# Optimization experiments

Measured on AMD Instinct MI355X. Metric: run time of the kernel, lower is better.

Reference implementation:

```python
import jax, jax.numpy as jnp
import numpy as np

ENC = 512            # encoder_image_size
RADIUS = 5.0         # user_input_circle_radius
B, Q, P = 4, 8, 4
IN_H, IN_W = 1024, 1024


def setup_inputs() -> dict:
    key = jax.random.key(0)
    k1, k2, k3 = jax.random.split(key, 3)
    batched_images = jax.random.uniform(k1, (B, 3, IN_H, IN_W), dtype=jnp.float32)
    # points in pixel coordinates of the input image
    batched_points = jax.random.uniform(k2, (B, Q, P, 2), dtype=jnp.float32) * jnp.float32(IN_W)
    batched_point_labels = jax.random.randint(k3, (B, Q, P), 0, 4, dtype=jnp.int32)
    pixel_mean = jnp.array([0.485, 0.456, 0.406], dtype=jnp.float32).reshape(1, 3, 1, 1)
    pixel_std = jnp.array([0.229, 0.224, 0.225], dtype=jnp.float32).reshape(1, 3, 1, 1)
    return {
        "batched_images": batched_images,
        "batched_points": batched_points,
        "batched_point_labels": batched_point_labels,
        "pixel_mean": pixel_mean,
        "pixel_std": pixel_std,
    }


def _early_fusion(batched_images, batched_points, batched_point_labels, pixel_mean, pixel_std):
    b, _, in_h, in_w = batched_images.shape
    q = batched_points.shape[1]
    S = ENC
    # preprocess: bilinear resize (align_corners=False) + normalize
    x = jax.image.resize(batched_images, (b, 3, S, S), method="bilinear", antialias=False)
    x = (x - pixel_mean) / pixel_std
    # rescale points to encoder resolution, keeping negatives at -1
    px = jnp.where(batched_points[..., 0] >= 0, batched_points[..., 0] * (S / in_w), -1.0)
    py = jnp.where(batched_points[..., 1] >= 0, batched_points[..., 1] * (S / in_h), -1.0)
    pts = jnp.stack([px, py], axis=-1)                      # [B,Q,P,2]

    rows = jnp.arange(S, dtype=jnp.float32)                 # row ids (y)
    cols = jnp.arange(S, dtype=jnp.float32)                 # col ids (x)

    # bbox mask from first two points if label[...,0] != 1, else full image
    is_bbox = (batched_point_labels[:, :, 0] != 1).astype(jnp.float32)   # [B,Q]
    tlx = is_bbox * jnp.min(pts[:, :, :2, 0], axis=-1)
    tly = is_bbox * jnp.min(pts[:, :, :2, 1], axis=-1)
    brx = is_bbox * jnp.max(pts[:, :, :2, 0], axis=-1) + (1.0 - is_bbox) * S
    bry = is_bbox * jnp.max(pts[:, :, :2, 1], axis=-1) + (1.0 - is_bbox) * S
    row_within = (rows[None, None, :, None] >= tly[:, :, None, None]) & (rows[None, None, :, None] <= bry[:, :, None, None])
    col_within = (cols[None, None, None, :] >= tlx[:, :, None, None]) & (cols[None, None, None, :] <= brx[:, :, None, None])
    bbox_mask = (row_within & col_within).astype(x.dtype)   # [B,Q,S,S]

    # point (circle) mask: min over points of squared distance, gated by label==1
    is_point = (batched_point_labels == 1).astype(jnp.float32)[:, :, None, None, :]   # [B,Q,1,1,P]
    dx = cols[None, None, None, :, None] - pts[:, :, None, None, :, 0]  # [B,Q,1,S,P]
    dy = rows[None, None, :, None, None] - pts[:, :, None, None, :, 1]  # [B,Q,S,1,P]
    d2 = dx * dx + dy * dy                                               # [B,Q,S,S,P]
    r2 = RADIUS * RADIUS
    gated = d2 * is_point + (1.0 - is_point) * (r2 + 1.0)
    pts_mask = (jnp.min(gated, axis=-1) <= r2).astype(x.dtype)          # [B,Q,S,S]

    imgs = jnp.broadcast_to(x[:, None], (b, q, 3, S, S))
    fused = jnp.concatenate([imgs, bbox_mask[:, :, None], pts_mask[:, :, None]], axis=2)
    return fused.reshape(b * q, 5, S, S)


def reference(batched_images, batched_points, batched_point_labels, pixel_mean, pixel_std):
    return _early_fusion(batched_images, batched_points, batched_point_labels, pixel_mean, pixel_std)
```

## Files before the change

### kernel.cpp

```cpp
#include <hip/hip_runtime.h>

#define S_ENC 512
#define IN_WH 1024
#define NB 4
#define NQ 8
#define NPTS 4

__global__ __launch_bounds__(256) void resize_norm_kernel(
    const float* __restrict__ img,
    const float* __restrict__ mean,
    const float* __restrict__ stdv,
    float* __restrict__ wimg)
{
  const int bc  = blockIdx.y;
  const int tid = blockIdx.x * 256 + threadIdx.x;
  const int y   = tid >> 7;
  const int x4  = (tid & 127) << 2;

  const float m = mean[bc % 3];
  const float s = stdv[bc % 3];

  const float* in0 = img + ((size_t)bc * IN_WH + (size_t)(2 * y)) * IN_WH + 2 * x4;
  const float4 a0 = *(const float4*)(in0);
  const float4 a1 = *(const float4*)(in0 + 4);
  const float4 b0 = *(const float4*)(in0 + IN_WH);
  const float4 b1 = *(const float4*)(in0 + IN_WH + 4);

  float4 r;
  r.x = 0.5f * (0.5f * (a0.x + a0.y) + 0.5f * (b0.x + b0.y));
  r.y = 0.5f * (0.5f * (a0.z + a0.w) + 0.5f * (b0.z + b0.w));
  r.z = 0.5f * (0.5f * (a1.x + a1.y) + 0.5f * (b1.x + b1.y));
  r.w = 0.5f * (0.5f * (a1.z + a1.w) + 0.5f * (b1.z + b1.w));
  r.x = (r.x - m) / s;
  r.y = (r.y - m) / s;
  r.z = (r.z - m) / s;
  r.w = (r.w - m) / s;

  *(float4*)(wimg + ((size_t)bc * S_ENC + y) * S_ENC + x4) = r;
}

template <bool UseWs>
__global__ __launch_bounds__(256) void fuse_kernel(
    const float* __restrict__ wimg,
    const float* __restrict__ img,
    const float* __restrict__ pts,
    const int*   __restrict__ labels,
    const float* __restrict__ mean,
    const float* __restrict__ stdv,
    float* __restrict__ out)
{
  const int plane = blockIdx.y;
  const int c  = plane % 5;
  const int bq = plane / 5;
  const int b  = bq >> 3;
  const int q  = bq & 7;

  const int tid = blockIdx.x * 256 + threadIdx.x;
  const int y   = tid >> 7;
  const int x4  = (tid & 127) << 2;

  float4 r;

  if (c < 3) {
    if (UseWs) {
      r = *(const float4*)(wimg + ((size_t)(b * 3 + c) * S_ENC + y) * S_ENC + x4);
    } else {
      const float m = mean[c];
      const float s = stdv[c];
      const float* in0 =
          img + ((size_t)(b * 3 + c) * IN_WH + (size_t)(2 * y)) * IN_WH + 2 * x4;
      const float4 a0 = *(const float4*)(in0);
      const float4 a1 = *(const float4*)(in0 + 4);
      const float4 b0 = *(const float4*)(in0 + IN_WH);
      const float4 b1 = *(const float4*)(in0 + IN_WH + 4);
      r.x = 0.5f * (0.5f * (a0.x + a0.y) + 0.5f * (b0.x + b0.y));
      r.y = 0.5f * (0.5f * (a0.z + a0.w) + 0.5f * (b0.z + b0.w));
      r.z = 0.5f * (0.5f * (a1.x + a1.y) + 0.5f * (b1.x + b1.y));
      r.w = 0.5f * (0.5f * (a1.z + a1.w) + 0.5f * (b1.z + b1.w));
      r.x = (r.x - m) / s;
      r.y = (r.y - m) / s;
      r.z = (r.z - m) / s;
      r.w = (r.w - m) / s;
    }
  } else {
    const float* p   = pts + (size_t)(bq) * NPTS * 2;
    const int*   lab = labels + (size_t)(bq) * NPTS;
    float px[NPTS], py[NPTS];
    int   lb[NPTS];
#pragma unroll
    for (int i = 0; i < NPTS; ++i) {
      const float vx = p[2 * i + 0];
      const float vy = p[2 * i + 1];
      px[i] = (vx >= 0.0f) ? __fmul_rn(vx, 0.5f) : -1.0f;
      py[i] = (vy >= 0.0f) ? __fmul_rn(vy, 0.5f) : -1.0f;
      lb[i] = lab[i];
    }
    const float fy = (float)y;
    float* rr = &r.x;

    if (c == 3) {
      float tlx, tly, brx, bry;
      if (lb[0] != 1) {
        tlx = fminf(px[0], px[1]);
        tly = fminf(py[0], py[1]);
        brx = fmaxf(px[0], px[1]);
        bry = fmaxf(py[0], py[1]);
      } else {
        tlx = 0.0f; tly = 0.0f;
        brx = (float)S_ENC; bry = (float)S_ENC;
      }
      const bool rowok = (fy >= tly) && (fy <= bry);
#pragma unroll
      for (int j = 0; j < 4; ++j) {
        const float fx = (float)(x4 + j);
        rr[j] = (rowok && fx >= tlx && fx <= brx) ? 1.0f : 0.0f;
      }
    } else {
#pragma unroll
      for (int j = 0; j < 4; ++j) {
        const float fx = (float)(x4 + j);
        float mind = 26.0f;
#pragma unroll
        for (int i = 0; i < NPTS; ++i) {
          if (lb[i] == 1) {
            const float dx = __fsub_rn(fx, px[i]);
            const float dy = __fsub_rn(fy, py[i]);
            const float d2 = __fadd_rn(__fmul_rn(dx, dx), __fmul_rn(dy, dy));
            mind = fminf(mind, d2);
          }
        }
        rr[j] = (mind <= 25.0f) ? 1.0f : 0.0f;
      }
    }
  }

  *(float4*)(out + ((size_t)plane * S_ENC + y) * S_ENC + x4) = r;
}

extern "C" void kernel_launch(void* const* d_in, const int* in_sizes, int n_in,
                              void* d_out, int out_size, void* d_ws, size_t ws_size,
                              hipStream_t stream) {
  const float* img    = (const float*)d_in[0];
  const float* pts    = (const float*)d_in[1];
  const int*   labels = (const int*)d_in[2];
  const float* mean   = (const float*)d_in[3];
  const float* stdv   = (const float*)d_in[4];
  float* out = (float*)d_out;

  const size_t ws_need = (size_t)NB * 3 * S_ENC * S_ENC * sizeof(float);

  if (d_ws != nullptr && ws_size >= ws_need) {
    float* wimg = (float*)d_ws;
    dim3 g1(256, NB * 3);
    resize_norm_kernel<<<g1, 256, 0, stream>>>(img, mean, stdv, wimg);
    dim3 g2(256, NB * NQ * 5);
    fuse_kernel<true><<<g2, 256, 0, stream>>>(wimg, img, pts, labels, mean, stdv, out);
  } else {
    dim3 g2(256, NB * NQ * 5);
    fuse_kernel<false><<<g2, 256, 0, stream>>>(nullptr, img, pts, labels, mean, stdv, out);
  }
}
```

Before: 39.94 us.

## Fuse resize and mask kernels, broadcast each resized plane to all queries

Replaces the two-kernel scheme (resize to a workspace, then a fuse kernel that re-reads it for every query) with one kernel. Image jobs compute each resized, normalized plane once and write it directly to all 8 query slots. Mask jobs compute the bbox and circle planes. This removes the workspace write and the per-query re-reads plus one launch. The cost is uneven work per block, since image blocks do 8 stores each.

```diff
diff --git a/kernel.cpp b/kernel.cpp
--- a/kernel.cpp
+++ b/kernel.cpp
@@ -5,43 +5,9 @@
 #define NB 4
 #define NQ 8
 #define NPTS 4
+#define PLANE_STRIDE (5 * S_ENC * S_ENC)
 
-__global__ __launch_bounds__(256) void resize_norm_kernel(
-    const float* __restrict__ img,
-    const float* __restrict__ mean,
-    const float* __restrict__ stdv,
-    float* __restrict__ wimg)
-{
-  const int bc  = blockIdx.y;
-  const int tid = blockIdx.x * 256 + threadIdx.x;
-  const int y   = tid >> 7;
-  const int x4  = (tid & 127) << 2;
-
-  const float m = mean[bc % 3];
-  const float s = stdv[bc % 3];
-
-  const float* in0 = img + ((size_t)bc * IN_WH + (size_t)(2 * y)) * IN_WH + 2 * x4;
-  const float4 a0 = *(const float4*)(in0);
-  const float4 a1 = *(const float4*)(in0 + 4);
-  const float4 b0 = *(const float4*)(in0 + IN_WH);
-  const float4 b1 = *(const float4*)(in0 + IN_WH + 4);
-
-  float4 r;
-  r.x = 0.5f * (0.5f * (a0.x + a0.y) + 0.5f * (b0.x + b0.y));
-  r.y = 0.5f * (0.5f * (a0.z + a0.w) + 0.5f * (b0.z + b0.w));
-  r.z = 0.5f * (0.5f * (a1.x + a1.y) + 0.5f * (b1.x + b1.y));
-  r.w = 0.5f * (0.5f * (a1.z + a1.w) + 0.5f * (b1.z + b1.w));
-  r.x = (r.x - m) / s;
-  r.y = (r.y - m) / s;
-  r.z = (r.z - m) / s;
-  r.w = (r.w - m) / s;
-
-  *(float4*)(wimg + ((size_t)bc * S_ENC + y) * S_ENC + x4) = r;
-}
-
-template <bool UseWs>
-__global__ __launch_bounds__(256) void fuse_kernel(
-    const float* __restrict__ wimg,
+__global__ __launch_bounds__(256) void early_fusion_kernel(
     const float* __restrict__ img,
     const float* __restrict__ pts,
     const int*   __restrict__ labels,
@@ -49,42 +15,48 @@
     const float* __restrict__ stdv,
     float* __restrict__ out)
 {
-  const int plane = blockIdx.y;
-  const int c  = plane % 5;
-  const int bq = plane / 5;
-  const int b  = bq >> 3;
-  const int q  = bq & 7;
-
+  const int job = blockIdx.y;
   const int tid = blockIdx.x * 256 + threadIdx.x;
   const int y   = tid >> 7;
   const int x4  = (tid & 127) << 2;
 
-  float4 r;
+  if (job < NB * 3) {
+    const int bc = job;
+    const int b  = bc / 3;
+    const int c  = bc % 3;
+    const float m = mean[c];
+    const float s = stdv[c];
 
-  if (c < 3) {
-    if (UseWs) {
-      r = *(const float4*)(wimg + ((size_t)(b * 3 + c) * S_ENC + y) * S_ENC + x4);
-    } else {
-      const float m = mean[c];
-      const float s = stdv[c];
-      const float* in0 =
-          img + ((size_t)(b * 3 + c) * IN_WH + (size_t)(2 * y)) * IN_WH + 2 * x4;
-      const float4 a0 = *(const float4*)(in0);
-      const float4 a1 = *(const float4*)(in0 + 4);
-      const float4 b0 = *(const float4*)(in0 + IN_WH);
-      const float4 b1 = *(const float4*)(in0 + IN_WH + 4);
-      r.x = 0.5f * (0.5f * (a0.x + a0.y) + 0.5f * (b0.x + b0.y));
-      r.y = 0.5f * (0.5f * (a0.z + a0.w) + 0.5f * (b0.z + b0.w));
-      r.z = 0.5f * (0.5f * (a1.x + a1.y) + 0.5f * (b1.x + b1.y));
-      r.w = 0.5f * (0.5f * (a1.z + a1.w) + 0.5f * (b1.z + b1.w));
-      r.x = (r.x - m) / s;
-      r.y = (r.y - m) / s;
-      r.z = (r.z - m) / s;
-      r.w = (r.w - m) / s;
+    const float* in0 =
+        img + ((size_t)bc * IN_WH + (size_t)(2 * y)) * IN_WH + 2 * x4;
+    const float4 a0 = *(const float4*)(in0);
+    const float4 a1 = *(const float4*)(in0 + 4);
+    const float4 b0 = *(const float4*)(in0 + IN_WH);
+    const float4 b1 = *(const float4*)(in0 + IN_WH + 4);
+
+    float4 r;
+    r.x = 0.5f * (0.5f * (a0.x + a0.y) + 0.5f * (b0.x + b0.y));
+    r.y = 0.5f * (0.5f * (a0.z + a0.w) + 0.5f * (b0.z + b0.w));
+    r.z = 0.5f * (0.5f * (a1.x + a1.y) + 0.5f * (b1.x + b1.y));
+    r.w = 0.5f * (0.5f * (a1.z + a1.w) + 0.5f * (b1.z + b1.w));
+    r.x = (r.x - m) / s;
+    r.y = (r.y - m) / s;
+    r.z = (r.z - m) / s;
+    r.w = (r.w - m) / s;
+
+    float* dst = out + ((size_t)(b * NQ * 5 + c) * S_ENC + y) * S_ENC + x4;
+#pragma unroll
+    for (int q = 0; q < NQ; ++q) {
+      *(float4*)(dst) = r;
+      dst += PLANE_STRIDE;
     }
   } else {
-    const float* p   = pts + (size_t)(bq) * NPTS * 2;
-    const int*   lab = labels + (size_t)(bq) * NPTS;
+    const int idx = job - NB * 3;
+    const int bq  = idx >> 1;
+    const int c   = 3 + (idx & 1);
+
+    const float* p   = pts + (size_t)bq * NPTS * 2;
+    const int*   lab = labels + (size_t)bq * NPTS;
     float px[NPTS], py[NPTS];
     int   lb[NPTS];
 #pragma unroll
@@ -96,6 +68,7 @@
       lb[i] = lab[i];
     }
     const float fy = (float)y;
+    float4 r;
     float* rr = &r.x;
 
     if (c == 3) {
@@ -132,9 +105,9 @@
         rr[j] = (mind <= 25.0f) ? 1.0f : 0.0f;
       }
     }
+
+    *(float4*)(out + ((size_t)(bq * 5 + c) * S_ENC + y) * S_ENC + x4) = r;
   }
-
-  *(float4*)(out + ((size_t)plane * S_ENC + y) * S_ENC + x4) = r;
 }
 
 extern "C" void kernel_launch(void* const* d_in, const int* in_sizes, int n_in,
@@ -147,16 +120,6 @@
   const float* stdv   = (const float*)d_in[4];
   float* out = (float*)d_out;
 
-  const size_t ws_need = (size_t)NB * 3 * S_ENC * S_ENC * sizeof(float);
-
-  if (d_ws != nullptr && ws_size >= ws_need) {
-    float* wimg = (float*)d_ws;
-    dim3 g1(256, NB * 3);
-    resize_norm_kernel<<<g1, 256, 0, stream>>>(img, mean, stdv, wimg);
-    dim3 g2(256, NB * NQ * 5);
-    fuse_kernel<true><<<g2, 256, 0, stream>>>(wimg, img, pts, labels, mean, stdv, out);
-  } else {
-    dim3 g2(256, NB * NQ * 5);
-    fuse_kernel<false><<<g2, 256, 0, stream>>>(nullptr, img, pts, labels, mean, stdv, out);
-  }
+  dim3 grid(256, NB * 3 + NB * NQ * 2);
+  early_fusion_kernel<<<grid, 256, 0, stream>>>(img, pts, labels, mean, stdv, out);
 }
```

Result: faster. 36.62 us (-8.3%).
